# Kernel tuning notes

Hardware: AMD Instinct MI355X
Metric: run time of the kernel (lower is better)

## Reference

```python
import jax, jax.numpy as jnp
import numpy as np

N_NODES = 100000
EMB_DIM = 128
N_LAYERS = 3
N_EDGES = 1600000


def setup_inputs() -> dict:
    key = jax.random.key(0)
    ks = jax.random.split(key, 6)
    edge_index = jax.random.randint(ks[0], (2, N_EDGES), 0, N_NODES, dtype=jnp.int32)
    deg_inv = jax.random.uniform(ks[1], (N_NODES,), dtype=jnp.float32)
    node_emb = 0.02 * jax.random.normal(ks[2], (N_NODES, EMB_DIM), dtype=jnp.float32)
    W = jax.random.normal(ks[3], (N_LAYERS, EMB_DIM, EMB_DIM), dtype=jnp.float32) / np.sqrt(EMB_DIM)
    b = jnp.zeros((N_LAYERS, EMB_DIM), dtype=jnp.float32)
    gamma = jnp.ones((EMB_DIM,), dtype=jnp.float32)
    beta = jnp.zeros((EMB_DIM,), dtype=jnp.float32)
    return {"edge_index": edge_index, "deg_inv": deg_inv, "node_emb": node_emb,
            "W": W, "b": b, "gamma": gamma, "beta": beta}


def reference(edge_index, deg_inv, node_emb, W, b, gamma, beta):
    src, dst = edge_index[0], edge_index[1]
    x = node_emb  # [N, d]
    for l in range(N_LAYERS):
        # scatter-add neighbor aggregation: m[v] = sum_{(u->v)} x[u]
        m = jax.ops.segment_sum(x[src], dst, num_segments=N_NODES)  # [N, d]
        m = m * deg_inv[:, None]
        h = jax.nn.gelu(m @ W[l] + b[l], approximate=False)  # dropout=0 (eval)
        x = x + h  # residual
    # LayerNorm over feature dim
    mu = jnp.mean(x, axis=-1, keepdims=True)
    var = jnp.var(x, axis=-1, keepdims=True)
    x = (x - mu) * jax.lax.rsqrt(var + 1e-5) * gamma + beta
    return x
```

## Files before the change

kernel.cpp:

```cpp
#include <hip/hip_runtime.h>
#include <hip/hip_bf16.h>
#include <math.h>

#define N_NODES 100000
#define EMB 128
#define N_EDGES 1600000
#define N_LAYERS 3

#define NB 400
#define NPB 250
#define CAP 8192
#define CAPB 6144
#define BSTR 16
#define EPT 8
#define BUCKET_THREADS 512
#define BUCKET_BLOCKS ((N_EDGES + BUCKET_THREADS * EPT - 1) / (BUCKET_THREADS * EPT))

typedef __bf16 bf16x8 __attribute__((ext_vector_type(8)));
typedef float f32x4 __attribute__((ext_vector_type(4)));


__global__ __launch_bounds__(BUCKET_THREADS) void bucket_kernel(
    const int* __restrict__ src, const int* __restrict__ dst,
    int* __restrict__ bcur, unsigned* __restrict__ pairs) {
  __shared__ int scnt[NB];
  __shared__ int sbase[NB];
  const int t = threadIdx.x;
  if (t < NB) scnt[t] = 0;
  __syncthreads();
  unsigned pk[EPT];
  int bk[EPT], lofs[EPT];
  const int base_e = blockIdx.x * BUCKET_THREADS * EPT;
#pragma unroll
  for (int it = 0; it < EPT; ++it) {
    int i = base_e + it * BUCKET_THREADS + t;
    bk[it] = -1;
    if (i < N_EDGES) {
      int d = dst[i];
      int s = src[i];
      int b = d / NPB;
      int vloc = d - b * NPB;
      bk[it] = b;
      pk[it] = ((unsigned)vloc << 17) | (unsigned)s;
      lofs[it] = atomicAdd(&scnt[b], 1);
    }
  }
  __syncthreads();
  if (t < NB) sbase[t] = atomicAdd(&bcur[t * BSTR], scnt[t]);
  __syncthreads();
#pragma unroll
  for (int it = 0; it < EPT; ++it) {
    if (bk[it] >= 0) {
      int idx = sbase[bk[it]] + lofs[it];
      if (idx < CAP) pairs[(size_t)bk[it] * CAP + idx] = pk[it];
    }
  }
}

__device__ __forceinline__ int* scan512(int* pin, int* pout, int t) {
  for (int off = 1; off < 512; off <<= 1) {
    for (int i = t; i < 512; i += 256) {
      int v = pin[i];
      if (i >= off) v += pin[i - off];
      pout[i] = v;
    }
    __syncthreads();
    int* tmp = pin; pin = pout; pout = tmp;
  }
  return pin;
}

__global__ __launch_bounds__(256) void fillb_kernel(const unsigned* __restrict__ pairs,
                                                    const int* __restrict__ bcur,
                                                    int* __restrict__ row_ptr,
                                                    int* __restrict__ col) {
  __shared__ int sA[512], sB[512];
  __shared__ int cnt[NPB], cur[NPB];
  __shared__ unsigned pstage[CAPB];
  __shared__ int colstage[CAPB];
  const int t = threadIdx.x;
  const int b = blockIdx.x;

  for (int i = t; i < 512; i += 256) sA[i] = (i < NB) ? bcur[i * BSTR] : 0;
  __syncthreads();
  int* r = scan512(sA, sB, t);
  int base_b = b ? r[b - 1] : 0;
  int n = r[b] - base_b;
  if (n > CAP) n = CAP;
  const unsigned* pg = pairs + (size_t)b * CAP;
  const bool fits = (n <= CAPB);

  if (fits) for (int i = t; i < n; i += 256) pstage[i] = pg[i];
  if (t < NPB) cnt[t] = 0;
  __syncthreads();
  for (int i = t; i < n; i += 256) atomicAdd(&cnt[(fits ? pstage[i] : pg[i]) >> 17], 1);
  __syncthreads();
  for (int i = t; i < 512; i += 256) sA[i] = (i < NPB) ? cnt[i] : 0;
  __syncthreads();
  r = scan512(sA, sB, t);
  if (t < NPB) {
    int ex = r[t] - cnt[t];
    row_ptr[b * NPB + t] = base_b + ex;
    cur[t] = ex;
  }
  if (b == NB - 1 && t == 0) row_ptr[N_NODES] = N_EDGES;
  __syncthreads();
  for (int i = t; i < n; i += 256) {
    unsigned p = fits ? pstage[i] : pg[i];
    int pos = atomicAdd(&cur[p >> 17], 1);
    int s = (int)(p & 0x1FFFFu);
    if (fits) colstage[pos] = s;
    else col[base_b + pos] = s;
  }
  __syncthreads();
  if (fits) for (int i = t; i < n; i += 256) col[base_b + i] = colstage[i];
}


__global__ __launch_bounds__(256) void tobf16_kernel(const float* __restrict__ in,
                                                     __hip_bfloat16* __restrict__ xb) {
  size_t i = (size_t)blockIdx.x * 256 + threadIdx.x;
  const float4* p = (const float4*)in + i * 2;
  float4 a = p[0], b = p[1];
  union { __hip_bfloat16 h[8]; uint4 u; } r;
  r.h[0] = __float2bfloat16(a.x); r.h[1] = __float2bfloat16(a.y);
  r.h[2] = __float2bfloat16(a.z); r.h[3] = __float2bfloat16(a.w);
  r.h[4] = __float2bfloat16(b.x); r.h[5] = __float2bfloat16(b.y);
  r.h[6] = __float2bfloat16(b.z); r.h[7] = __float2bfloat16(b.w);
  ((uint4*)xb)[i] = r.u;
}

__global__ __launch_bounds__(256) void wt_kernel(const float* __restrict__ W,
                                                 __hip_bfloat16* __restrict__ WT) {
  int l = blockIdx.x;
  const float* Wl = W + (size_t)l * EMB * EMB;
  __hip_bfloat16* WTl = WT + (size_t)l * EMB * EMB;
  for (int i = threadIdx.x; i < EMB * EMB; i += 256) {
    int k = i >> 7, c = i & 127;
    WTl[c * EMB + k] = __float2bfloat16(Wl[i]);
  }
}


__device__ __forceinline__ float bf_lo(unsigned int w) { return __uint_as_float(w << 16); }
__device__ __forceinline__ float bf_hi(unsigned int w) { return __uint_as_float(w & 0xFFFF0000u); }

__device__ __forceinline__ float gelu_exact(float v) {
  return 0.5f * v * (1.f + erff(v * 0.70710678118654752f));
}

template <int LAST>
__global__ __launch_bounds__(1024, 8) void fused_kernel(
    const __hip_bfloat16* __restrict__ xb_in,
    const int* __restrict__ row_ptr,
    const int* __restrict__ col,
    const float* __restrict__ deg_inv,
    const __hip_bfloat16* __restrict__ WTl,
    const float* __restrict__ bias,
    __hip_bfloat16* __restrict__ xb_out,
    float* __restrict__ xf_out,
    const float* __restrict__ gamma,
    const float* __restrict__ beta) {
  __shared__ __hip_bfloat16 sM[16][136];

  const int t = threadIdx.x;
  const int w = t >> 6;
  const int lane = t & 63;
  const int q = lane >> 4;
  const int l15 = lane & 15;
  const int row0b = blockIdx.x * 16;

  const char* gbase = (const char*)xb_in + l15 * 16;
  {
    const int v = __builtin_amdgcn_readfirstlane(row0b + w);
    const int beg = row_ptr[v], end = row_ptr[v + 1];
    float a0 = 0.f, a1 = 0.f, a2 = 0.f, a3 = 0.f, a4 = 0.f, a5 = 0.f, a6 = 0.f, a7 = 0.f;
#define ACC8(W) { a0 += bf_lo(W.x); a1 += bf_hi(W.x); a2 += bf_lo(W.y); a3 += bf_hi(W.y); \
                  a4 += bf_lo(W.z); a5 += bf_hi(W.z); a6 += bf_lo(W.w); a7 += bf_hi(W.w); }
    int e = beg;
    for (; e + 16 <= end; e += 16) {
      int u0 = col[e + q];
      int u1 = col[e + 4 + q];
      int u2 = col[e + 8 + q];
      int u3 = col[e + 12 + q];
      uint4 w0 = *(const uint4*)(gbase + (size_t)u0 * 256);
      uint4 w1 = *(const uint4*)(gbase + (size_t)u1 * 256);
      uint4 w2 = *(const uint4*)(gbase + (size_t)u2 * 256);
      uint4 w3 = *(const uint4*)(gbase + (size_t)u3 * 256);
      ACC8(w0) ACC8(w1) ACC8(w2) ACC8(w3)
    }
    for (; e < end; e += 4) {
      int idx = e + q;
      bool valid = idx < end;
      int u = col[valid ? idx : beg];
      uint4 w0 = *(const uint4*)(gbase + (size_t)u * 256);
      if (valid) ACC8(w0)
    }
#undef ACC8
    a0 += __shfl_xor(a0, 16, 64); a0 += __shfl_xor(a0, 32, 64);
    a1 += __shfl_xor(a1, 16, 64); a1 += __shfl_xor(a1, 32, 64);
    a2 += __shfl_xor(a2, 16, 64); a2 += __shfl_xor(a2, 32, 64);
    a3 += __shfl_xor(a3, 16, 64); a3 += __shfl_xor(a3, 32, 64);
    a4 += __shfl_xor(a4, 16, 64); a4 += __shfl_xor(a4, 32, 64);
    a5 += __shfl_xor(a5, 16, 64); a5 += __shfl_xor(a5, 32, 64);
    a6 += __shfl_xor(a6, 16, 64); a6 += __shfl_xor(a6, 32, 64);
    a7 += __shfl_xor(a7, 16, 64); a7 += __shfl_xor(a7, 32, 64);
    if (q == 0) {
      float di = deg_inv[v];
      union { __hip_bfloat16 h[8]; uint4 u4; } r;
      r.h[0] = __float2bfloat16(a0 * di); r.h[1] = __float2bfloat16(a1 * di);
      r.h[2] = __float2bfloat16(a2 * di); r.h[3] = __float2bfloat16(a3 * di);
      r.h[4] = __float2bfloat16(a4 * di); r.h[5] = __float2bfloat16(a5 * di);
      r.h[6] = __float2bfloat16(a6 * di); r.h[7] = __float2bfloat16(a7 * di);
      *(uint4*)(&sM[w][l15 * 8]) = r.u4;
    }
  }

  bf16x8 bfr[4];
  if (w < 8) {
    const __hip_bfloat16* wp = WTl + (size_t)(w * 16 + l15) * EMB + q * 8;
#pragma unroll
    for (int ks = 0; ks < 4; ++ks)
      bfr[ks] = *(const bf16x8*)(wp + ks * 32);
  }
  __syncthreads();

  f32x4 acc = (f32x4)(0.f);
  if (w < 8) {
#pragma unroll
    for (int ks = 0; ks < 4; ++ks) {
      bf16x8 af = *(const bf16x8*)(&sM[l15][q * 8 + ks * 32]);
      acc = __builtin_amdgcn_mfma_f32_16x16x32_bf16(af, bfr[ks], acc, 0, 0, 0);
    }
  }
  __syncthreads();
  if (w < 8) {
    const int colg = w * 16 + l15;
    const float bb = bias[colg];
#pragma unroll
    for (int j = 0; j < 4; ++j)
      sM[q * 4 + j][colg] = __float2bfloat16(gelu_exact(acc[j] + bb));
  }
  __syncthreads();

  {
    const size_t rowoff = (size_t)(row0b + w) * EMB;
    unsigned rg = *(const unsigned*)(&sM[w][lane * 2]);
    unsigned rr = *(const unsigned*)((const char*)xb_in + (rowoff + lane * 2) * 2);
    float v1 = bf_lo(rr) + bf_lo(rg);
    float v2 = bf_hi(rr) + bf_hi(rg);
    if (!LAST) {
      union { __hip_bfloat16 h[2]; unsigned u; } o;
      o.h[0] = __float2bfloat16(v1);
      o.h[1] = __float2bfloat16(v2);
      *(unsigned*)((char*)xb_out + (rowoff + lane * 2) * 2) = o.u;
    } else {
      float s = v1 + v2;
      float sq = fmaf(v1, v1, v2 * v2);
      for (int off = 1; off < 64; off <<= 1) {
        s += __shfl_xor(s, off, 64);
        sq += __shfl_xor(sq, off, 64);
      }
      float mu = s * (1.f / EMB);
      float var = sq * (1.f / EMB) - mu * mu;
      float rstd = rsqrtf(var + 1e-5f);
      float2 g = *(const float2*)(gamma + lane * 2);
      float2 be = *(const float2*)(beta + lane * 2);
      float2 o;
      o.x = (v1 - mu) * rstd * g.x + be.x;
      o.y = (v2 - mu) * rstd * g.y + be.y;
      *(float2*)(xf_out + rowoff + lane * 2) = o;
    }
  }
}


extern "C" void kernel_launch(void* const* d_in, const int* in_sizes, int n_in,
                              void* d_out, int out_size, void* d_ws, size_t ws_size,
                              hipStream_t stream) {
  const int* edge_index = (const int*)d_in[0];
  const float* deg_inv = (const float*)d_in[1];
  const float* node_emb = (const float*)d_in[2];
  const float* W = (const float*)d_in[3];
  const float* b = (const float*)d_in[4];
  const float* gamma = (const float*)d_in[5];
  const float* beta = (const float*)d_in[6];
  const int* src = edge_index;
  const int* dst = edge_index + N_EDGES;
  float* x = (float*)d_out;

  char* ws = (char*)d_ws;
  auto take = [&](size_t bytes) {
    char* p = ws;
    ws += (bytes + 255) & ~(size_t)255;
    return p;
  };
  __hip_bfloat16* xbA = (__hip_bfloat16*)take((size_t)N_NODES * EMB * 2);
  __hip_bfloat16* xbB = (__hip_bfloat16*)take((size_t)N_NODES * EMB * 2);
  __hip_bfloat16* WT = (__hip_bfloat16*)take((size_t)N_LAYERS * EMB * EMB * 2);
  int* row_ptr = (int*)take((N_NODES + 1) * sizeof(int));
  int* col = (int*)take(N_EDGES * sizeof(int));
  int* bcur = (int*)take(NB * BSTR * sizeof(int));
  unsigned* pairs = (unsigned*)xbB;

  hipMemsetAsync(bcur, 0, NB * BSTR * sizeof(int), stream);

  tobf16_kernel<<<N_NODES * EMB / 8 / 256, 256, 0, stream>>>(node_emb, xbA);
  wt_kernel<<<N_LAYERS, 256, 0, stream>>>(W, WT);

  bucket_kernel<<<BUCKET_BLOCKS, BUCKET_THREADS, 0, stream>>>(src, dst, bcur, pairs);
  fillb_kernel<<<NB, 256, 0, stream>>>(pairs, bcur, row_ptr, col);

  const int NBLK = N_NODES / 16;
  fused_kernel<0><<<NBLK, 1024, 0, stream>>>(xbA, row_ptr, col, deg_inv,
                                             WT, b, xbB, nullptr, nullptr, nullptr);
  fused_kernel<0><<<NBLK, 1024, 0, stream>>>(xbB, row_ptr, col, deg_inv,
                                             WT + (size_t)EMB * EMB, b + EMB,
                                             xbA, nullptr, nullptr, nullptr);
  fused_kernel<1><<<NBLK, 1024, 0, stream>>>(xbA, row_ptr, col, deg_inv,
                                             WT + (size_t)2 * EMB * EMB, b + 2 * EMB,
                                             nullptr, x, gamma, beta);
}
```

Measured before the change: 328.9 us.

## Split fused aggregate+GEMM kernel into separate aggregation and GEMM kernels

The per-layer fused kernel is split into two kernels. A gather-aggregate kernel uses 256-thread blocks, one wave per node, and writes the normalized messages to a new bf16 global buffer. A GEMM+GELU+residual kernel then reads that buffer directly into MFMA operands. The aim is to decouple the latency-bound gather from the 1024-thread block's barriers and the idle waves during the matmul, which should improve occupancy and load balance. The cost is an extra global write and read of a 25.6 MB buffer per layer, plus three more kernel launches.

```diff
diff --git a/kernel.cpp b/kernel.cpp
--- a/kernel.cpp
+++ b/kernel.cpp
@@ -149,12 +149,67 @@
   return 0.5f * v * (1.f + erff(v * 0.70710678118654752f));
 }
 
-template <int LAST>
-__global__ __launch_bounds__(1024, 8) void fused_kernel(
+__global__ __launch_bounds__(256, 8) void aggregate_kernel(
     const __hip_bfloat16* __restrict__ xb_in,
     const int* __restrict__ row_ptr,
     const int* __restrict__ col,
     const float* __restrict__ deg_inv,
+    __hip_bfloat16* __restrict__ mb) {
+  const int t = threadIdx.x;
+  const int lane = t & 63;
+  const int q = lane >> 4;
+  const int l15 = lane & 15;
+  const int v = __builtin_amdgcn_readfirstlane((blockIdx.x * 256 + t) >> 6);
+  if (v >= N_NODES) return;
+
+  const char* gbase = (const char*)xb_in + l15 * 16;
+  const int beg = row_ptr[v], end = row_ptr[v + 1];
+  float a0 = 0.f, a1 = 0.f, a2 = 0.f, a3 = 0.f, a4 = 0.f, a5 = 0.f, a6 = 0.f, a7 = 0.f;
+#define ACC8(W) { a0 += bf_lo(W.x); a1 += bf_hi(W.x); a2 += bf_lo(W.y); a3 += bf_hi(W.y); \
+                  a4 += bf_lo(W.z); a5 += bf_hi(W.z); a6 += bf_lo(W.w); a7 += bf_hi(W.w); }
+  int e = beg;
+  for (; e + 16 <= end; e += 16) {
+    int u0 = col[e + q];
+    int u1 = col[e + 4 + q];
+    int u2 = col[e + 8 + q];
+    int u3 = col[e + 12 + q];
+    uint4 w0 = *(const uint4*)(gbase + (size_t)u0 * 256);
+    uint4 w1 = *(const uint4*)(gbase + (size_t)u1 * 256);
+    uint4 w2 = *(const uint4*)(gbase + (size_t)u2 * 256);
+    uint4 w3 = *(const uint4*)(gbase + (size_t)u3 * 256);
+    ACC8(w0) ACC8(w1) ACC8(w2) ACC8(w3)
+  }
+  for (; e < end; e += 4) {
+    int idx = e + q;
+    bool valid = idx < end;
+    int u = col[valid ? idx : beg];
+    uint4 w0 = *(const uint4*)(gbase + (size_t)u * 256);
+    if (valid) ACC8(w0)
+  }
+#undef ACC8
+  a0 += __shfl_xor(a0, 16, 64); a0 += __shfl_xor(a0, 32, 64);
+  a1 += __shfl_xor(a1, 16, 64); a1 += __shfl_xor(a1, 32, 64);
+  a2 += __shfl_xor(a2, 16, 64); a2 += __shfl_xor(a2, 32, 64);
+  a3 += __shfl_xor(a3, 16, 64); a3 += __shfl_xor(a3, 32, 64);
+  a4 += __shfl_xor(a4, 16, 64); a4 += __shfl_xor(a4, 32, 64);
+  a5 += __shfl_xor(a5, 16, 64); a5 += __shfl_xor(a5, 32, 64);
+  a6 += __shfl_xor(a6, 16, 64); a6 += __shfl_xor(a6, 32, 64);
+  a7 += __shfl_xor(a7, 16, 64); a7 += __shfl_xor(a7, 32, 64);
+  if (q == 0) {
+    float di = deg_inv[v];
+    union { __hip_bfloat16 h[8]; uint4 u4; } r;
+    r.h[0] = __float2bfloat16(a0 * di); r.h[1] = __float2bfloat16(a1 * di);
+    r.h[2] = __float2bfloat16(a2 * di); r.h[3] = __float2bfloat16(a3 * di);
+    r.h[4] = __float2bfloat16(a4 * di); r.h[5] = __float2bfloat16(a5 * di);
+    r.h[6] = __float2bfloat16(a6 * di); r.h[7] = __float2bfloat16(a7 * di);
+    *(uint4*)((char*)mb + (size_t)v * 256 + l15 * 16) = r.u4;
+  }
+}
+
+template <int LAST>
+__global__ __launch_bounds__(1024, 8) void gemm_kernel(
+    const __hip_bfloat16* __restrict__ mb,
+    const __hip_bfloat16* __restrict__ xb_in,
     const __hip_bfloat16* __restrict__ WTl,
     const float* __restrict__ bias,
     __hip_bfloat16* __restrict__ xb_out,
@@ -170,71 +225,20 @@
   const int l15 = lane & 15;
   const int row0b = blockIdx.x * 16;
 
-  const char* gbase = (const char*)xb_in + l15 * 16;
-  {
-    const int v = __builtin_amdgcn_readfirstlane(row0b + w);
-    const int beg = row_ptr[v], end = row_ptr[v + 1];
-    float a0 = 0.f, a1 = 0.f, a2 = 0.f, a3 = 0.f, a4 = 0.f, a5 = 0.f, a6 = 0.f, a7 = 0.f;
-#define ACC8(W) { a0 += bf_lo(W.x); a1 += bf_hi(W.x); a2 += bf_lo(W.y); a3 += bf_hi(W.y); \
-                  a4 += bf_lo(W.z); a5 += bf_hi(W.z); a6 += bf_lo(W.w); a7 += bf_hi(W.w); }
-    int e = beg;
-    for (; e + 16 <= end; e += 16) {
-      int u0 = col[e + q];
-      int u1 = col[e + 4 + q];
-      int u2 = col[e + 8 + q];
-      int u3 = col[e + 12 + q];
-      uint4 w0 = *(const uint4*)(gbase + (size_t)u0 * 256);
-      uint4 w1 = *(const uint4*)(gbase + (size_t)u1 * 256);
-      uint4 w2 = *(const uint4*)(gbase + (size_t)u2 * 256);
-      uint4 w3 = *(const uint4*)(gbase + (size_t)u3 * 256);
-      ACC8(w0) ACC8(w1) ACC8(w2) ACC8(w3)
-    }
-    for (; e < end; e += 4) {
-      int idx = e + q;
-      bool valid = idx < end;
-      int u = col[valid ? idx : beg];
-      uint4 w0 = *(const uint4*)(gbase + (size_t)u * 256);
-      if (valid) ACC8(w0)
-    }
-#undef ACC8
-    a0 += __shfl_xor(a0, 16, 64); a0 += __shfl_xor(a0, 32, 64);
-    a1 += __shfl_xor(a1, 16, 64); a1 += __shfl_xor(a1, 32, 64);
-    a2 += __shfl_xor(a2, 16, 64); a2 += __shfl_xor(a2, 32, 64);
-    a3 += __shfl_xor(a3, 16, 64); a3 += __shfl_xor(a3, 32, 64);
-    a4 += __shfl_xor(a4, 16, 64); a4 += __shfl_xor(a4, 32, 64);
-    a5 += __shfl_xor(a5, 16, 64); a5 += __shfl_xor(a5, 32, 64);
-    a6 += __shfl_xor(a6, 16, 64); a6 += __shfl_xor(a6, 32, 64);
-    a7 += __shfl_xor(a7, 16, 64); a7 += __shfl_xor(a7, 32, 64);
-    if (q == 0) {
-      float di = deg_inv[v];
-      union { __hip_bfloat16 h[8]; uint4 u4; } r;
-      r.h[0] = __float2bfloat16(a0 * di); r.h[1] = __float2bfloat16(a1 * di);
-      r.h[2] = __float2bfloat16(a2 * di); r.h[3] = __float2bfloat16(a3 * di);
-      r.h[4] = __float2bfloat16(a4 * di); r.h[5] = __float2bfloat16(a5 * di);
-      r.h[6] = __float2bfloat16(a6 * di); r.h[7] = __float2bfloat16(a7 * di);
-      *(uint4*)(&sM[w][l15 * 8]) = r.u4;
-    }
-  }
-
-  bf16x8 bfr[4];
   if (w < 8) {
+    bf16x8 bfr[4];
     const __hip_bfloat16* wp = WTl + (size_t)(w * 16 + l15) * EMB + q * 8;
 #pragma unroll
     for (int ks = 0; ks < 4; ++ks)
       bfr[ks] = *(const bf16x8*)(wp + ks * 32);
-  }
-  __syncthreads();
-
-  f32x4 acc = (f32x4)(0.f);
-  if (w < 8) {
+
+    const __hip_bfloat16* ap = mb + (size_t)(row0b + l15) * EMB + q * 8;
+    f32x4 acc = (f32x4)(0.f);
 #pragma unroll
     for (int ks = 0; ks < 4; ++ks) {
-      bf16x8 af = *(const bf16x8*)(&sM[l15][q * 8 + ks * 32]);
+      bf16x8 af = *(const bf16x8*)(ap + ks * 32);
       acc = __builtin_amdgcn_mfma_f32_16x16x32_bf16(af, bfr[ks], acc, 0, 0, 0);
     }
-  }
-  __syncthreads();
-  if (w < 8) {
     const int colg = w * 16 + l15;
     const float bb = bias[colg];
 #pragma unroll
@@ -297,11 +301,12 @@
   };
   __hip_bfloat16* xbA = (__hip_bfloat16*)take((size_t)N_NODES * EMB * 2);
   __hip_bfloat16* xbB = (__hip_bfloat16*)take((size_t)N_NODES * EMB * 2);
+  __hip_bfloat16* mb = (__hip_bfloat16*)take((size_t)N_NODES * EMB * 2);
   __hip_bfloat16* WT = (__hip_bfloat16*)take((size_t)N_LAYERS * EMB * EMB * 2);
   int* row_ptr = (int*)take((N_NODES + 1) * sizeof(int));
   int* col = (int*)take(N_EDGES * sizeof(int));
   int* bcur = (int*)take(NB * BSTR * sizeof(int));
-  unsigned* pairs = (unsigned*)xbB;
+  unsigned* pairs = (unsigned*)mb;
 
   hipMemsetAsync(bcur, 0, NB * BSTR * sizeof(int), stream);
 
@@ -311,13 +316,18 @@
   bucket_kernel<<<BUCKET_BLOCKS, BUCKET_THREADS, 0, stream>>>(src, dst, bcur, pairs);
   fillb_kernel<<<NB, 256, 0, stream>>>(pairs, bcur, row_ptr, col);
 
-  const int NBLK = N_NODES / 16;
-  fused_kernel<0><<<NBLK, 1024, 0, stream>>>(xbA, row_ptr, col, deg_inv,
-                                             WT, b, xbB, nullptr, nullptr, nullptr);
-  fused_kernel<0><<<NBLK, 1024, 0, stream>>>(xbB, row_ptr, col, deg_inv,
-                                             WT + (size_t)EMB * EMB, b + EMB,
-                                             xbA, nullptr, nullptr, nullptr);
-  fused_kernel<1><<<NBLK, 1024, 0, stream>>>(xbA, row_ptr, col, deg_inv,
-                                             WT + (size_t)2 * EMB * EMB, b + 2 * EMB,
-                                             nullptr, x, gamma, beta);
-}
+  const int AGG_BLOCKS = (N_NODES + 3) / 4;
+  const int GEMM_BLOCKS = N_NODES / 16;
+
+  aggregate_kernel<<<AGG_BLOCKS, 256, 0, stream>>>(xbA, row_ptr, col, deg_inv, mb);
+  gemm_kernel<0><<<GEMM_BLOCKS, 1024, 0, stream>>>(mb, xbA, WT, b, xbB,
+                                                   nullptr, nullptr, nullptr);
+  aggregate_kernel<<<AGG_BLOCKS, 256, 0, stream>>>(xbB, row_ptr, col, deg_inv, mb);
+  gemm_kernel<0><<<GEMM_BLOCKS, 1024, 0, stream>>>(mb, xbB, WT + (size_t)EMB * EMB,
+                                                   b + EMB, xbA,
+                                                   nullptr, nullptr, nullptr);
+  aggregate_kernel<<<AGG_BLOCKS, 256, 0, stream>>>(xbA, row_ptr, col, deg_inv, mb);
+  gemm_kernel<1><<<GEMM_BLOCKS, 1024, 0, stream>>>(mb, xbA, WT + (size_t)2 * EMB * EMB,
+                                                   b + 2 * EMB, nullptr,
+                                                   x, gamma, beta);
+}
```

Result: slower. 417.2 us (+26.9%).
